# Optimization experiments

Measured on AMD Instinct MI355X. Metric: run time of the kernel, lower is better.

## Reference

```python
import jax, jax.numpy as jnp
import numpy as np

PAD, BOS, EOS = 0, 1, 2
VOCAB, EMB, HID, BATCH, MAXLEN = 32, 64, 1024, 2048, 100


def setup_inputs() -> dict:
    key = jax.random.key(0)
    ks = jax.random.split(key, 11)
    s = 0.08  # small init scale keeps softmax/sigmoid in a sane range
    g = lambda k, shape: (s * jax.random.normal(k, shape)).astype(jnp.float32)
    emb = g(ks[0], (VOCAB, EMB)).at[PAD].set(0.0)  # padding_idx row = 0
    return {
        "prevs": jnp.full((BATCH, 1), BOS, dtype=jnp.int32),
        "emb": emb,
        "Wih0": g(ks[1], (4 * HID, EMB)),
        "Whh0": g(ks[2], (4 * HID, HID)),
        "bih0": g(ks[3], (4 * HID,)),
        "bhh0": g(ks[4], (4 * HID,)),
        "Wih1": g(ks[5], (4 * HID, HID)),
        "Whh1": g(ks[6], (4 * HID, HID)),
        "bih1": g(ks[7], (4 * HID,)),
        "bhh1": g(ks[8], (4 * HID,)),
        "Wout": g(ks[9], (VOCAB, HID)),
        "bout": g(ks[10], (VOCAB,)),
        "max_len": MAXLEN,
    }


def _lstm_cell(x, h, c, Wih, Whh, bih, bhh):
    # torch LSTM gate order: i, f, g, o
    gates = x @ Wih.T + bih + h @ Whh.T + bhh  # [n, 4H]
    i, f, g, o = jnp.split(gates, 4, axis=-1)
    c = jax.nn.sigmoid(f) * c + jax.nn.sigmoid(i) * jnp.tanh(g)
    h = jax.nn.sigmoid(o) * jnp.tanh(c)
    return h, c


def reference(prevs, emb, Wih0, Whh0, bih0, bhh0, Wih1, Whh1, bih1, bhh1,
              Wout, bout, max_len):
    n = prevs.shape[0]
    H = Whh0.shape[1]
    prev = prevs[:, 0].astype(jnp.int32)
    h0 = jnp.zeros((n, H), jnp.float32)
    c0 = jnp.zeros((n, H), jnp.float32)
    h1 = jnp.zeros((n, H), jnp.float32)
    c1 = jnp.zeros((n, H), jnp.float32)
    is_end = prev == EOS
    lengths = jnp.zeros((n,), jnp.int32)
    keys = jax.random.split(jax.random.key(42), max_len)

    def step(carry, k):
        prev, h0, c0, h1, c1, is_end, lengths = carry
        x = emb[prev]                                   # [n, E]
        h0, c0 = _lstm_cell(x, h0, c0, Wih0, Whh0, bih0, bhh0)
        h1, c1 = _lstm_cell(h0, h1, c1, Wih1, Whh1, bih1, bhh1)
        logits = h1 @ Wout.T + bout                     # [n, V]
        cur = jax.random.categorical(k, logits).astype(jnp.int32)
        cur = jnp.where(is_end, PAD, cur)               # finished rows emit PAD
        lengths = lengths + (~is_end).astype(jnp.int32)
        is_end = is_end | (cur == EOS)
        return (cur, h0, c0, h1, c1, is_end, lengths), cur

    carry, seq = jax.lax.scan(step, (prev, h0, c0, h1, c1, is_end, lengths), keys)
    lengths = carry[6] + 1                               # +1 for BOS, as in sample_tensor
    sequences = jnp.concatenate([prevs.astype(jnp.int32), seq.T], axis=1)  # [n, 1+max_len]
    return sequences, lengths
```

## Files before the change

kernel.cpp:

```cpp
#include <hip/hip_runtime.h>
#include <cstdint>
#include <cstddef>


constexpr int PAD_TOK = 0, BOS_TOK = 1, EOS_TOK = 2;
constexpr int VOCAB = 32, EMB = 64, HID = 1024, BATCH = 2048, MAXLEN = 100;
constexpr int BK = 32;
constexpr int NKT_H = HID / BK;
constexpr float SCALE = 64.0f;
constexpr double INV_S2 = 1.0 / 4096.0;

using half8 = __attribute__((ext_vector_type(8))) _Float16;
using f32x4 = __attribute__((ext_vector_type(4))) float;
typedef unsigned short u16;
typedef uint32_t u32;

__device__ __forceinline__ u32 rotl32(u32 v, int d) {
  return (v << d) | (v >> (32 - d));
}

__device__ __forceinline__ void threefry2x32(u32 k0, u32 k1, u32 x0, u32 x1,
                                             u32& y0, u32& y1) {
  const u32 k2 = k0 ^ k1 ^ 0x1BD11BDAu;
#define TF_ROUND(r) do { x0 += x1; x1 = rotl32(x1, (r)); x1 ^= x0; } while (0)
  x0 += k0; x1 += k1;
  TF_ROUND(13); TF_ROUND(15); TF_ROUND(26); TF_ROUND(6);
  x0 += k1; x1 += k2 + 1u;
  TF_ROUND(17); TF_ROUND(29); TF_ROUND(16); TF_ROUND(24);
  x0 += k2; x1 += k0 + 2u;
  TF_ROUND(13); TF_ROUND(15); TF_ROUND(26); TF_ROUND(6);
  x0 += k0; x1 += k1 + 3u;
  TF_ROUND(17); TF_ROUND(29); TF_ROUND(16); TF_ROUND(24);
  x0 += k1; x1 += k2 + 4u;
  TF_ROUND(13); TF_ROUND(15); TF_ROUND(26); TF_ROUND(6);
  x0 += k2; x1 += k0 + 5u;
#undef TF_ROUND
  y0 = x0; y1 = x1;
}

__device__ __forceinline__ void gl_lds16(const void* g, void* l) {
  __builtin_amdgcn_global_load_lds(
      (const __attribute__((address_space(1))) void*)g,
      (__attribute__((address_space(3))) void*)l, 16, 0, 0);
}

__device__ __forceinline__ double rcp1p(double q) {
  const double d = 1.0 + q;
  double r = (double)__builtin_amdgcn_rcpf((float)d);
  r = r * fma(-d, r, 2.0);
  r = r * fma(-d, r, 2.0);
  return r;
}
__device__ __forceinline__ double exp2d(double t) {
  const double n = rint(t);
  const double f = t - n;
  double p = 1.0178086009239699e-07;
  p = fma(p, f, 1.3215542443841225e-06);
  p = fma(p, f, 1.5252733804059840e-05);
  p = fma(p, f, 1.5403530393381610e-04);
  p = fma(p, f, 1.3333558146428443e-03);
  p = fma(p, f, 9.6181291076284772e-03);
  p = fma(p, f, 5.5504108664821580e-02);
  p = fma(p, f, 2.4022650695910071e-01);
  p = fma(p, f, 6.9314718055994531e-01);
  p = fma(p, f, 1.0);
  const long long e = ((long long)(int)n + 1023) << 52;
  return p * __longlong_as_double(e);
}
__device__ __forceinline__ double sigd(double x) {
  return rcp1p(exp2d(x * -1.4426950408889634));
}
__device__ __forceinline__ double tanhd(double x) {
  return fma(2.0, rcp1p(exp2d(x * -2.8853900817779268)), -1.0);
}

__global__ __launch_bounds__(256) void pack_w(
    const float* __restrict__ src, int K, int nkt,
    uint4* __restrict__ dhi, uint4* __restrict__ dlo, int nchunks) {
  const int g = blockIdx.x * 256 + threadIdx.x;
  if (g >= nchunks) return;
  const int ut = g / (nkt * 512);
  const int rem = g - ut * (nkt * 512);
  const int kt = rem >> 9;
  const int slot = rem & 511;
  const int fm = slot >> 6, kg = (slot >> 4) & 3, r15 = slot & 15;
  const int row = (fm & 3) * HID + ut * 32 + (fm >> 2) * 16 + r15;
  const int col = kt * 32 + kg * 8;
  const float* s = src + (size_t)row * K + col;
  u16 hh[8], ll[8];
#pragma unroll
  for (int e = 0; e < 8; ++e) {
    const float x = s[e] * SCALE;
    const _Float16 h = (_Float16)x;
    const float rm = x - (float)h;
    const _Float16 l = (_Float16)rm;
    hh[e] = __builtin_bit_cast(u16, h);
    ll[e] = __builtin_bit_cast(u16, l);
  }
  dhi[g] = make_uint4((u32)hh[0] | ((u32)hh[1] << 16),
                      (u32)hh[2] | ((u32)hh[3] << 16),
                      (u32)hh[4] | ((u32)hh[5] << 16),
                      (u32)hh[6] | ((u32)hh[7] << 16));
  dlo[g] = make_uint4((u32)ll[0] | ((u32)ll[1] << 16),
                      (u32)ll[2] | ((u32)ll[3] << 16),
                      (u32)ll[4] | ((u32)ll[5] << 16),
                      (u32)ll[6] | ((u32)ll[7] << 16));
}

__global__ __launch_bounds__(256) void split_kernel(
    const float* __restrict__ src, u16* __restrict__ hi, u16* __restrict__ lo,
    int n) {
  const int i = blockIdx.x * 256 + threadIdx.x;
  if (i >= n) return;
  const float x = src[i] * SCALE;
  const _Float16 h = (_Float16)x;
  const float rem = x - (float)h;
  const _Float16 l = (_Float16)rem;
  hi[i] = __builtin_bit_cast(u16, h);
  lo[i] = __builtin_bit_cast(u16, l);
}

__global__ __launch_bounds__(256) void init_kernel(
    const int* __restrict__ prevs, float* __restrict__ c0,
    float* __restrict__ c1, u16* __restrict__ h0hi0, u16* __restrict__ h0lo0,
    u16* __restrict__ h0hi1, u16* __restrict__ h0lo1,
    u16* __restrict__ h1hi0, u16* __restrict__ h1lo0,
    u16* __restrict__ h1hi1, u16* __restrict__ h1lo1,
    int* __restrict__ prev, int* __restrict__ is_end,
    int* __restrict__ lengths, u32* __restrict__ keys,
    int* __restrict__ out_tok) {
  const int tid = blockIdx.x * 256 + threadIdx.x;
  const int total = BATCH * HID;
  if (tid < total) {
    c0[tid] = 0.0f; c1[tid] = 0.0f;
    h0hi0[tid] = 0; h0lo0[tid] = 0; h0hi1[tid] = 0; h0lo1[tid] = 0;
    h1hi0[tid] = 0; h1lo0[tid] = 0; h1hi1[tid] = 0; h1lo1[tid] = 0;
  }
  if (tid < BATCH) {
    const int p = prevs[tid];
    prev[tid] = p;
    is_end[tid] = (p == EOS_TOK) ? 1 : 0;
    lengths[tid] = 0;
    out_tok[(size_t)tid * (MAXLEN + 1)] = p;
  }
  if (tid < MAXLEN) {
    u32 y0, y1;
    threefry2x32(0u, 42u, 0u, (u32)tid, y0, y1);
    keys[2 * tid] = y0;
    keys[2 * tid + 1] = y1;
  }
}

template <bool GATHER, bool WRITE_F32>
__global__ __launch_bounds__(512, 2) void lstm_mfma(
    const uint4* __restrict__ A0p_hi, const uint4* __restrict__ A0p_lo,
    const u16* __restrict__ Ehi, const u16* __restrict__ Elo,
    const int* __restrict__ ptok, int nk0,
    const uint4* __restrict__ A1p_hi, const uint4* __restrict__ A1p_lo,
    const uint4* __restrict__ W0hi, const uint4* __restrict__ W0lo,
    const uint4* __restrict__ W1hi, const uint4* __restrict__ W1lo,
    const float* __restrict__ bih, const float* __restrict__ bhh,
    float* __restrict__ Cst, float* __restrict__ Hf32,
    uint4* __restrict__ Hp_hi, uint4* __restrict__ Hp_lo) {
  __shared__ uint4 lds4[2560];
  char* lds = (char*)lds4;

  const int tid = threadIdx.x;
  const int lane = tid & 63;
  const int wid = tid >> 6;
  const int wm = wid >> 1, wn = wid & 1;

  const int bid = blockIdx.x;
  const int swz = (bid & 7) * 32 + (bid >> 3);
  const int ut = swz >> 3;
  const int mt = swz & 7;
  const int u0 = ut * 32;
  const int row0 = mt * 256;

  const int r15 = lane & 15;
  const int kgrp = lane >> 4;

  int tok4[4];
  if (GATHER) {
#pragma unroll
    for (int mi = 0; mi < 4; ++mi)
      tok4[mi] = ptok[row0 + (wm * 4 + mi) * 16 + r15];
  }

  const int NT = nk0 + NKT_H;

  auto ldsW = [&](int buf, int pl, int slot) -> char* {
    return lds + buf * 16384 + pl * 8192 + slot * 16;
  };

  auto stageW = [&](int buf, int kt) {
    const bool s0 = kt < nk0;
    const int ktl = s0 ? kt : kt - nk0;
    const uint4* wh = s0 ? W0hi : W1hi;
    const uint4* wl = s0 ? W0lo : W1lo;
    const int wbase = (ut * (s0 ? nk0 : NKT_H) + ktl) * 512 + wid * 64;
    gl_lds16(wh + wbase + lane, ldsW(buf, 0, wid * 64));
    gl_lds16(wl + wbase + lane, ldsW(buf, 1, wid * 64));
  };

  auto loadA = [&](int kt, uint4* Ah, uint4* Al) {
    const bool s0 = kt < nk0;
    const int ktl = s0 ? kt : kt - nk0;
    if (GATHER && s0) {
#pragma unroll
      for (int mi = 0; mi < 4; ++mi) {
        const size_t ao = (size_t)tok4[mi] * EMB + ktl * 32 + kgrp * 8;
        Ah[mi] = *(const uint4*)(Ehi + ao);
        Al[mi] = *(const uint4*)(Elo + ao);
      }
    } else {
      const uint4* ah_ = s0 ? A0p_hi : A1p_hi;
      const uint4* al_ = s0 ? A0p_lo : A1p_lo;
      const int ab = (mt * NKT_H + ktl) * 1024 + wm * 256 + lane;
#pragma unroll
      for (int mi = 0; mi < 4; ++mi) {
        Ah[mi] = ah_[ab + mi * 64];
        Al[mi] = al_[ab + mi * 64];
      }
    }
  };

  f32x4 acc[4][4] = {};

  auto compute = [&](const uint4* AhF, const uint4* AlF, int buf) {
    half8 ah[4], al[4];
#pragma unroll
    for (int mi = 0; mi < 4; ++mi) {
      ah[mi] = __builtin_bit_cast(half8, AhF[mi]);
      al[mi] = __builtin_bit_cast(half8, AlF[mi]);
    }
#pragma unroll
    for (int ni = 0; ni < 4; ++ni) {
      const half8 bh = *(const half8*)ldsW(buf, 0, (wn * 4 + ni) * 64 + lane);
      const half8 bl = *(const half8*)ldsW(buf, 1, (wn * 4 + ni) * 64 + lane);
#pragma unroll
      for (int mi = 0; mi < 4; ++mi) {
        acc[mi][ni] =
            __builtin_amdgcn_mfma_f32_16x16x32_f16(ah[mi], bh, acc[mi][ni], 0, 0, 0);
        acc[mi][ni] =
            __builtin_amdgcn_mfma_f32_16x16x32_f16(ah[mi], bl, acc[mi][ni], 0, 0, 0);
        acc[mi][ni] =
            __builtin_amdgcn_mfma_f32_16x16x32_f16(al[mi], bh, acc[mi][ni], 0, 0, 0);
      }
    }
  };

  uint4 Ah0[4], Al0[4], Ah1[4], Al1[4];
  loadA(0, Ah0, Al0);
  stageW(0, 0);
  __syncthreads();
#pragma unroll 1
  for (int t = 0; t < NT; t += 2) {
    loadA(t + 1, Ah1, Al1);
    stageW(1, t + 1);
    compute(Ah0, Al0, 0);
    __syncthreads();
    if (t + 2 < NT) {
      loadA(t + 2, Ah0, Al0);
      stageW(0, t + 2);
    }
    compute(Ah1, Al1, 1);
    __syncthreads();
  }

  const int u_loc = wn * 16 + r15;
  const int u = u0 + u_loc;
  double bsum[4];
#pragma unroll
  for (int g = 0; g < 4; ++g)
    bsum[g] = (double)bih[g * HID + u] + (double)bhh[g * HID + u];

  float* Cb = Cst + (size_t)(mt * 32 + ut) * 8192;
  u16* hhT = (u16*)lds;
  u16* hlT = (u16*)(lds + 20480);
  const int hi4 = lane >> 4;

#pragma unroll
  for (int mi = 0; mi < 4; ++mi) {
#pragma unroll
    for (int r = 0; r < 4; ++r) {
      const int row = wm * 64 + mi * 16 + hi4 * 4 + r;
      const double gI = (double)acc[mi][0][r] * INV_S2 + bsum[0];
      const double gF = (double)acc[mi][1][r] * INV_S2 + bsum[1];
      const double gG = (double)acc[mi][2][r] * INV_S2 + bsum[2];
      const double gO = (double)acc[mi][3][r] * INV_S2 + bsum[3];
      const double ii = sigd(gI);
      const double ff = sigd(gF);
      const double gt = tanhd(gG);
      const double oo = sigd(gO);
      const int co = row * 32 + u_loc;
      const double cn = ff * (double)Cb[co] + ii * gt;
      Cb[co] = (float)cn;
      const float hf = (float)(oo * tanhd(cn));
      if (WRITE_F32) Hf32[(size_t)(row0 + row) * HID + u] = hf;
      const float hs = hf * SCALE;
      const _Float16 hh = (_Float16)hs;
      const float rm = hs - (float)hh;
      const _Float16 hl = (_Float16)rm;
      hhT[row * 40 + u_loc] = __builtin_bit_cast(u16, hh);
      hlT[row * 40 + u_loc] = __builtin_bit_cast(u16, hl);
    }
  }
  __syncthreads();

  const size_t mtut = ((size_t)mt * NKT_H + ut) * 1024;
#pragma unroll
  for (int j = 0; j < 2; ++j) {
    const int g = tid + j * 512;
    const int fA = g >> 6, kg = (g >> 4) & 3, rr = g & 15;
    const int row = fA * 16 + rr;
    const uint4 vh = *(const uint4*)(hhT + row * 40 + kg * 8);
    const uint4 vl = *(const uint4*)(hlT + row * 40 + kg * 8);
    Hp_hi[mtut + g] = vh;
    Hp_lo[mtut + g] = vl;
  }
}

__global__ __launch_bounds__(256) void sample_kernel(
    const float* __restrict__ h1, const float* __restrict__ Wout,
    const float* __restrict__ bout, const u32* __restrict__ keys, int t,
    int* __restrict__ prev, int* __restrict__ is_end, int* __restrict__ lengths,
    int* __restrict__ out_tok, int* __restrict__ len_out) {
  const int wave = threadIdx.x >> 6;
  const int lane = threadIdx.x & 63;
  const int row = blockIdx.x * 4 + wave;
  const int v = lane & 31;
  const int half = lane >> 5;

  const float* hseg = h1 + (size_t)row * HID + half * (HID / 2);
  const float* wseg = Wout + (size_t)v * HID + half * (HID / 2);

  double acc = 0.0;
#pragma unroll 4
  for (int k = 0; k < HID / 2; k += 4) {
    const float4 w = *(const float4*)(wseg + k);
    const float4 h = *(const float4*)(hseg + k);
    acc = fma((double)w.x, (double)h.x, acc);
    acc = fma((double)w.y, (double)h.y, acc);
    acc = fma((double)w.z, (double)h.z, acc);
    acc = fma((double)w.w, (double)h.w, acc);
  }
  acc += __shfl_xor(acc, 32);

  const u32 k0 = keys[2 * t], k1 = keys[2 * t + 1];
  u32 y0, y1;
  threefry2x32(k0, k1, 0u, (u32)(row * VOCAB + v), y0, y1);
  const u32 bits = y0 ^ y1;
  const float f = __uint_as_float((bits >> 9) | 0x3f800000u) - 1.0f;
  const float uu = fmaxf(f, 1.17549435e-38f);
  const double g = -log(-log((double)uu));

  double z = acc + (double)bout[v] + g;
  int idx = v;
#pragma unroll
  for (int m = 1; m < 32; m <<= 1) {
    const double zo = __shfl_xor(z, m);
    const int io = __shfl_xor(idx, m);
    if (zo > z || (zo == z && io < idx)) { z = zo; idx = io; }
  }

  if (lane == 0) {
    const int e = is_end[row];
    const int cur = e ? PAD_TOK : idx;
    const int len = lengths[row] + (e ? 0 : 1);
    const int enew = e | (cur == EOS_TOK ? 1 : 0);
    prev[row] = cur;
    is_end[row] = enew;
    lengths[row] = len;
    out_tok[(size_t)row * (MAXLEN + 1) + t + 1] = cur;
    if (len_out) len_out[row] = len + 1;
  }
}

extern "C" void kernel_launch(void* const* d_in, const int* in_sizes, int n_in,
                              void* d_out, int out_size, void* d_ws,
                              size_t ws_size, hipStream_t stream) {
  const int* prevs = (const int*)d_in[0];
  const float* emb = (const float*)d_in[1];
  const float* Wih0 = (const float*)d_in[2];
  const float* Whh0 = (const float*)d_in[3];
  const float* bih0 = (const float*)d_in[4];
  const float* bhh0 = (const float*)d_in[5];
  const float* Wih1 = (const float*)d_in[6];
  const float* Whh1 = (const float*)d_in[7];
  const float* bih1 = (const float*)d_in[8];
  const float* bhh1 = (const float*)d_in[9];
  const float* Wout = (const float*)d_in[10];
  const float* bout = (const float*)d_in[11];

  const size_t SH = (size_t)BATCH * HID;
  const size_t CH = SH / 8;
  const size_t CW = (size_t)32 * NKT_H * 512;
  const size_t CW0 = (size_t)32 * 2 * 512;

  float* c0 = (float*)d_ws;
  float* c1 = c0 + SH;
  float* h1f = c1 + SH;
  uint4* q = (uint4*)(h1f + SH);
  uint4* ph0hi[2] = {q, q + CH};
  uint4* ph0lo[2] = {q + 2 * CH, q + 3 * CH};
  uint4* ph1hi[2] = {q + 4 * CH, q + 5 * CH};
  uint4* ph1lo[2] = {q + 6 * CH, q + 7 * CH};
  uint4* pw = q + 8 * CH;
  uint4* pwih0h = pw;              uint4* pwih0l = pwih0h + CW0;
  uint4* pwhh0h = pwih0l + CW0;    uint4* pwhh0l = pwhh0h + CW;
  uint4* pwih1h = pwhh0l + CW;     uint4* pwih1l = pwih1h + CW;
  uint4* pwhh1h = pwih1l + CW;     uint4* pwhh1l = pwhh1h + CW;
  u16* embh = (u16*)(pwhh1l + CW);
  u16* embl = embh + VOCAB * EMB;
  int* prev = (int*)(embl + VOCAB * EMB);
  int* is_end = prev + BATCH;
  int* lengths = is_end + BATCH;
  u32* keys = (u32*)(lengths + BATCH);

  int* out_tok = (int*)d_out;
  int* len_out = out_tok + (size_t)BATCH * (MAXLEN + 1);

  init_kernel<<<dim3((BATCH * HID) / 256), 256, 0, stream>>>(
      prevs, c0, c1, (u16*)ph0hi[0], (u16*)ph0lo[0], (u16*)ph0hi[1],
      (u16*)ph0lo[1], (u16*)ph1hi[0], (u16*)ph1lo[0], (u16*)ph1hi[1],
      (u16*)ph1lo[1], prev, is_end, lengths, keys, out_tok);

  split_kernel<<<dim3((VOCAB * EMB + 255) / 256), 256, 0, stream>>>(
      emb, embh, embl, VOCAB * EMB);
  pack_w<<<dim3((int)((CW0 + 255) / 256)), 256, 0, stream>>>(
      Wih0, EMB, 2, pwih0h, pwih0l, (int)CW0);
  pack_w<<<dim3((int)((CW + 255) / 256)), 256, 0, stream>>>(
      Whh0, HID, NKT_H, pwhh0h, pwhh0l, (int)CW);
  pack_w<<<dim3((int)((CW + 255) / 256)), 256, 0, stream>>>(
      Wih1, HID, NKT_H, pwih1h, pwih1l, (int)CW);
  pack_w<<<dim3((int)((CW + 255) / 256)), 256, 0, stream>>>(
      Whh1, HID, NKT_H, pwhh1h, pwhh1l, (int)CW);

  int p = 0;
  for (int t = 0; t < MAXLEN; ++t) {
    lstm_mfma<true, false><<<dim3(256), 512, 0, stream>>>(
        nullptr, nullptr, embh, embl, prev, 2, ph0hi[p], ph0lo[p],
        pwih0h, pwih0l, pwhh0h, pwhh0l, bih0, bhh0, c0, nullptr,
        ph0hi[p ^ 1], ph0lo[p ^ 1]);
    lstm_mfma<false, true><<<dim3(256), 512, 0, stream>>>(
        ph0hi[p ^ 1], ph0lo[p ^ 1], nullptr, nullptr, nullptr, NKT_H,
        ph1hi[p], ph1lo[p], pwih1h, pwih1l, pwhh1h, pwhh1l, bih1, bhh1,
        c1, h1f, ph1hi[p ^ 1], ph1lo[p ^ 1]);
    sample_kernel<<<dim3(BATCH / 4), 256, 0, stream>>>(
        h1f, Wout, bout, keys, t, prev, is_end, lengths, out_tok,
        (t == MAXLEN - 1) ? len_out : nullptr);
    p ^= 1;
  }
  (void)in_sizes; (void)n_in; (void)out_size; (void)ws_size;
}
```

Measured before the change: 18.63 ms.

## Load weight tiles directly to registers, drop LDS staging and barriers

Measured after the change: 21.00 ms. 12.7% more time.

```diff
diff --git a/kernel.cpp b/kernel.cpp
--- a/kernel.cpp
+++ b/kernel.cpp
@@ -38,12 +38,6 @@
   y0 = x0; y1 = x1;
 }
 
-__device__ __forceinline__ void gl_lds16(const void* g, void* l) {
-  __builtin_amdgcn_global_load_lds(
-      (const __attribute__((address_space(1))) void*)g,
-      (__attribute__((address_space(3))) void*)l, 16, 0, 0);
-}
-
 __device__ __forceinline__ double rcp1p(double q) {
   const double d = 1.0 + q;
   double r = (double)__builtin_amdgcn_rcpf((float)d);
@@ -171,9 +165,8 @@
   const int wm = wid >> 1, wn = wid & 1;
 
   const int bid = blockIdx.x;
-  const int swz = (bid & 7) * 32 + (bid >> 3);
-  const int ut = swz >> 3;
-  const int mt = swz & 7;
+  const int mt = bid & 7;
+  const int ut = bid >> 3;
   const int u0 = ut * 32;
   const int row0 = mt * 256;
 
@@ -189,23 +182,17 @@
 
   const int NT = nk0 + NKT_H;
 
-  auto ldsW = [&](int buf, int pl, int slot) -> char* {
-    return lds + buf * 16384 + pl * 8192 + slot * 16;
-  };
-
-  auto stageW = [&](int buf, int kt) {
+  auto loadT = [&](int kt, uint4* Ah, uint4* Al, uint4* Bh, uint4* Bl) {
     const bool s0 = kt < nk0;
     const int ktl = s0 ? kt : kt - nk0;
     const uint4* wh = s0 ? W0hi : W1hi;
     const uint4* wl = s0 ? W0lo : W1lo;
-    const int wbase = (ut * (s0 ? nk0 : NKT_H) + ktl) * 512 + wid * 64;
-    gl_lds16(wh + wbase + lane, ldsW(buf, 0, wid * 64));
-    gl_lds16(wl + wbase + lane, ldsW(buf, 1, wid * 64));
-  };
-
-  auto loadA = [&](int kt, uint4* Ah, uint4* Al) {
-    const bool s0 = kt < nk0;
-    const int ktl = s0 ? kt : kt - nk0;
+    const int wb = (ut * (s0 ? nk0 : NKT_H) + ktl) * 512 + wn * 256 + lane;
+#pragma unroll
+    for (int ni = 0; ni < 4; ++ni) {
+      Bh[ni] = wh[wb + ni * 64];
+      Bl[ni] = wl[wb + ni * 64];
+    }
     if (GATHER && s0) {
 #pragma unroll
       for (int mi = 0; mi < 4; ++mi) {
@@ -227,45 +214,46 @@
 
   f32x4 acc[4][4] = {};
 
-  auto compute = [&](const uint4* AhF, const uint4* AlF, int buf) {
-    half8 ah[4], al[4];
-#pragma unroll
-    for (int mi = 0; mi < 4; ++mi) {
-      ah[mi] = __builtin_bit_cast(half8, AhF[mi]);
-      al[mi] = __builtin_bit_cast(half8, AlF[mi]);
+  auto computeT = [&](const uint4* AhF, const uint4* AlF, const uint4* BhF,
+                      const uint4* BlF) {
+    half8 ah[4], al[4], bh[4], bl[4];
+#pragma unroll
+    for (int i = 0; i < 4; ++i) {
+      ah[i] = __builtin_bit_cast(half8, AhF[i]);
+      al[i] = __builtin_bit_cast(half8, AlF[i]);
+      bh[i] = __builtin_bit_cast(half8, BhF[i]);
+      bl[i] = __builtin_bit_cast(half8, BlF[i]);
     }
 #pragma unroll
-    for (int ni = 0; ni < 4; ++ni) {
-      const half8 bh = *(const half8*)ldsW(buf, 0, (wn * 4 + ni) * 64 + lane);
-      const half8 bl = *(const half8*)ldsW(buf, 1, (wn * 4 + ni) * 64 + lane);
-#pragma unroll
-      for (int mi = 0; mi < 4; ++mi) {
-        acc[mi][ni] =
-            __builtin_amdgcn_mfma_f32_16x16x32_f16(ah[mi], bh, acc[mi][ni], 0, 0, 0);
-        acc[mi][ni] =
-            __builtin_amdgcn_mfma_f32_16x16x32_f16(ah[mi], bl, acc[mi][ni], 0, 0, 0);
-        acc[mi][ni] =
-            __builtin_amdgcn_mfma_f32_16x16x32_f16(al[mi], bh, acc[mi][ni], 0, 0, 0);
-      }
-    }
+    for (int ni = 0; ni < 4; ++ni)
+#pragma unroll
+      for (int mi = 0; mi < 4; ++mi)
+        acc[mi][ni] = __builtin_amdgcn_mfma_f32_16x16x32_f16(
+            ah[mi], bh[ni], acc[mi][ni], 0, 0, 0);
+#pragma unroll
+    for (int ni = 0; ni < 4; ++ni)
+#pragma unroll
+      for (int mi = 0; mi < 4; ++mi)
+        acc[mi][ni] = __builtin_amdgcn_mfma_f32_16x16x32_f16(
+            ah[mi], bl[ni], acc[mi][ni], 0, 0, 0);
+#pragma unroll
+    for (int ni = 0; ni < 4; ++ni)
+#pragma unroll
+      for (int mi = 0; mi < 4; ++mi)
+        acc[mi][ni] = __builtin_amdgcn_mfma_f32_16x16x32_f16(
+            al[mi], bh[ni], acc[mi][ni], 0, 0, 0);
   };
 
-  uint4 Ah0[4], Al0[4], Ah1[4], Al1[4];
-  loadA(0, Ah0, Al0);
-  stageW(0, 0);
-  __syncthreads();
+  uint4 Ah0[4], Al0[4], Bh0[4], Bl0[4];
+  uint4 Ah1[4], Al1[4], Bh1[4], Bl1[4];
+  loadT(0, Ah0, Al0, Bh0, Bl0);
+  loadT(1, Ah1, Al1, Bh1, Bl1);
 #pragma unroll 1
   for (int t = 0; t < NT; t += 2) {
-    loadA(t + 1, Ah1, Al1);
-    stageW(1, t + 1);
-    compute(Ah0, Al0, 0);
-    __syncthreads();
-    if (t + 2 < NT) {
-      loadA(t + 2, Ah0, Al0);
-      stageW(0, t + 2);
-    }
-    compute(Ah1, Al1, 1);
-    __syncthreads();
+    computeT(Ah0, Al0, Bh0, Bl0);
+    if (t + 2 < NT) loadT(t + 2, Ah0, Al0, Bh0, Bl0);
+    computeT(Ah1, Al1, Bh1, Bl1);
+    if (t + 3 < NT) loadT(t + 3, Ah1, Al1, Bh1, Bl1);
   }
 
   const int u_loc = wn * 16 + r15;
@@ -328,7 +316,7 @@
     int* __restrict__ out_tok, int* __restrict__ len_out) {
   const int wave = threadIdx.x >> 6;
   const int lane = threadIdx.x & 63;
-  const int row = blockIdx.x * 4 + wave;
+  const int row = (blockIdx.x & 7) * 256 + (blockIdx.x >> 3) * 4 + wave;
   const int v = lane & 31;
   const int half = lane >> 5;
 
```
